# Kernel optimization log

Hardware: AMD Instinct MI355X
Metric: run time of the kernel (lower is better)

The kernel has to match this reference:

```python
import jax, jax.numpy as jnp
import numpy as np

IDENTITY_WEIGHT = 0.5
EPS_NORM = 1e-6   # channel RMSNorm eps
EPS_COS = 1e-12   # cosine-sim norm eps (matches torch F.normalize default)


def setup_inputs() -> dict:
    key = jax.random.key(0)
    k1, k2 = jax.random.split(key)
    B, C, H, W = 32, 768, 32, 32
    X = jax.random.normal(k1, (B, C, H, W), dtype=jnp.float32)
    # 1x1 conv weight [out=3C, in=C] (kernel dims squeezed)
    W_in = jax.random.normal(k2, (3 * C, C), dtype=jnp.float32) * (C ** -0.5)
    return {"X": X, "W_in": W_in}


def _cos_sim(t):
    # normalize over the flattened spatial axis (last dim)
    return t / (jnp.linalg.norm(t, axis=-1, keepdims=True) + EPS_COS)


def reference(X, W_in):
    B, C, H, W = X.shape
    # norm: parameter-free RMS over channel dim
    Xn = X * jax.lax.rsqrt(jnp.mean(X * X, axis=1, keepdims=True) + EPS_NORM)
    # 1x1 conv (bias-free) == channel GEMM: [B,3C,H,W]
    qkv = jnp.einsum('oc,bchw->bohw', W_in, Xn)
    K = qkv[:, :C].reshape(B, 1, C, H * W)       # b h c (x y), h=1
    V = qkv[:, C:2 * C].reshape(B, 1, C, H * W)
    # cosine similarity per channel over spatial positions: [B,1,C,1]
    A = jnp.sum(_cos_sim(K) * _cos_sim(V), axis=-1, keepdims=True)
    # affine gate with identity weight (feature_map_attn = identity)
    A = (1.0 - IDENTITY_WEIGHT) * A + IDENTITY_WEIGHT
    A = A.reshape(B, C, 1, 1)  # 'b 1 c 1 -> b c 1 1'
    return A * X
```

## Files before the change

### kernel.cpp

```cpp
#include <hip/hip_runtime.h>
#include <hip/hip_bf16.h>
#include <cstdint>
#include <cstddef>


#define B_   32
#define C_   768
#define HW_  1024
#define CHW_ (C_ * HW_)
#define EPS_NORM 1e-6f
#define EPS_COS  1e-12f

using f32x4  = __attribute__((ext_vector_type(4))) float;
using bf16x8 = __attribute__((ext_vector_type(8))) short;

__device__ inline unsigned short f2bf(float f) {
    union { float f; unsigned u; } v; v.f = f;
    unsigned u = v.u;
    u += 0x7fffu + ((u >> 16) & 1u);
    return (unsigned short)(u >> 16);
}

__global__ void sumsq_kernel(const float* __restrict__ X, float* __restrict__ ssum) {
    const int b  = blockIdx.z;
    const int hw = blockIdx.y * 256 + threadIdx.x;
    const int c0 = blockIdx.x * 128;
    const float* xp = X + (size_t)b * CHW_ + (size_t)c0 * HW_ + hw;
    float s = 0.f;
    #pragma unroll 8
    for (int c = 0; c < 128; ++c) {
        float v = xp[(size_t)c * HW_];
        s += v * v;
    }
    atomicAdd(&ssum[b * HW_ + hw], s);
}

__global__ void wconv_kernel(const float* __restrict__ W, unsigned short* __restrict__ Wbf) {
    const int i = blockIdx.x * 256 + threadIdx.x;
    const float4 v = reinterpret_cast<const float4*>(W)[i];
    ushort4 o;
    o.x = f2bf(v.x); o.y = f2bf(v.y); o.z = f2bf(v.z); o.w = f2bf(v.w);
    reinterpret_cast<ushort4*>(Wbf)[i] = o;
}

__global__ void xnt_kernel(const float* __restrict__ X, const float* __restrict__ ssum,
                           unsigned short* __restrict__ Xnt) {
    const int b   = blockIdx.z;
    const int c0  = blockIdx.y * 64;
    const int hw0 = blockIdx.x * 64;
    const int tid = threadIdx.x;
    __shared__ short T[64][72];

    #pragma unroll
    for (int it = 0; it < 4; ++it) {
        int q  = it * 256 + tid;
        int r  = q >> 4;
        int c4 = (q & 15) * 4;
        const float4 x = *reinterpret_cast<const float4*>(
            X + (size_t)b * CHW_ + (size_t)(c0 + r) * HW_ + hw0 + c4);
        const float4 s = *reinterpret_cast<const float4*>(ssum + b * HW_ + hw0 + c4);
        ushort4 o;
        o.x = f2bf(x.x * rsqrtf(s.x * (1.f / 768.f) + EPS_NORM));
        o.y = f2bf(x.y * rsqrtf(s.y * (1.f / 768.f) + EPS_NORM));
        o.z = f2bf(x.z * rsqrtf(s.z * (1.f / 768.f) + EPS_NORM));
        o.w = f2bf(x.w * rsqrtf(s.w * (1.f / 768.f) + EPS_NORM));
        *reinterpret_cast<ushort4*>(&T[r][c4]) = o;
    }
    __syncthreads();
    #pragma unroll
    for (int it = 0; it < 2; ++it) {
        int q  = it * 256 + tid;
        int rp = q >> 3;
        int cc = (q & 7) * 8;
        __align__(16) unsigned short tmp[8];
        #pragma unroll
        for (int j = 0; j < 8; ++j) tmp[j] = (unsigned short)T[cc + j][rp];
        *reinterpret_cast<uint4*>(
            Xnt + (size_t)b * CHW_ + (size_t)(hw0 + rp) * C_ + c0 + cc) =
            *reinterpret_cast<const uint4*>(tmp);
    }
}

__global__ __launch_bounds__(256, 2) void gemm_kernel(
        const unsigned short* __restrict__ Wbf,
        const unsigned short* __restrict__ Xnt,
        float* __restrict__ wsA) {
    const int n0   = blockIdx.x * 128;
    const int c0   = blockIdx.y * 128;
    const int b    = blockIdx.z;
    const int tid  = threadIdx.x;
    const int lane = tid & 63;
    const int wave = tid >> 6;
    const int wm   = (wave >> 1) * 64;
    const int wn   = (wave & 1) * 64;
    const int quad = lane >> 4;
    const int l15  = lane & 15;

    __shared__ short sAK[128][40];
    __shared__ short sAV[128][40];
    __shared__ short sB [128][40];

    const f32x4 zero = {0.f, 0.f, 0.f, 0.f};
    f32x4 accK[4][4], accV[4][4];
    #pragma unroll
    for (int i = 0; i < 4; ++i)
        #pragma unroll
        for (int j = 0; j < 4; ++j) { accK[i][j] = zero; accV[i][j] = zero; }

    const size_t wk_base = (size_t)c0 * 768;
    const size_t wv_base = (size_t)(768 + c0) * 768;
    const size_t xb      = (size_t)b * CHW_ + (size_t)n0 * 768;

    for (int k0 = 0; k0 < 768; k0 += 32) {
        __syncthreads();
        #pragma unroll
        for (int it = 0; it < 2; ++it) {
            int chunk = it * 256 + tid;
            int r  = chunk >> 2;
            int kk = (chunk & 3) * 8;
            uint4 vk = *reinterpret_cast<const uint4*>(Wbf + wk_base + (size_t)r * 768 + k0 + kk);
            *reinterpret_cast<uint4*>(&sAK[r][kk]) = vk;
            uint4 vv = *reinterpret_cast<const uint4*>(Wbf + wv_base + (size_t)r * 768 + k0 + kk);
            *reinterpret_cast<uint4*>(&sAV[r][kk]) = vv;
            uint4 vb = *reinterpret_cast<const uint4*>(Xnt + xb + (size_t)r * 768 + k0 + kk);
            *reinterpret_cast<uint4*>(&sB[r][kk]) = vb;
        }
        __syncthreads();

        bf16x8 aK[4], aV[4], bF[4];
        #pragma unroll
        for (int i = 0; i < 4; ++i) {
            aK[i] = *reinterpret_cast<const bf16x8*>(&sAK[wm + 16 * i + l15][quad * 8]);
            aV[i] = *reinterpret_cast<const bf16x8*>(&sAV[wm + 16 * i + l15][quad * 8]);
            bF[i] = *reinterpret_cast<const bf16x8*>(&sB [wn + 16 * i + l15][quad * 8]);
        }
        #pragma unroll
        for (int i = 0; i < 4; ++i)
            #pragma unroll
            for (int j = 0; j < 4; ++j) {
                accK[i][j] = __builtin_amdgcn_mfma_f32_16x16x32_bf16(aK[i], bF[j], accK[i][j], 0, 0, 0);
                accV[i][j] = __builtin_amdgcn_mfma_f32_16x16x32_bf16(aV[i], bF[j], accV[i][j], 0, 0, 0);
            }
    }

    #pragma unroll
    for (int i = 0; i < 4; ++i) {
        #pragma unroll
        for (int r = 0; r < 4; ++r) {
            float pd = 0.f, pk = 0.f, pv = 0.f;
            #pragma unroll
            for (int j = 0; j < 4; ++j) {
                float kk = accK[i][j][r], vv = accV[i][j][r];
                pd += kk * vv; pk += kk * kk; pv += vv * vv;
            }
            #pragma unroll
            for (int off = 1; off < 16; off <<= 1) {
                pd += __shfl_xor(pd, off);
                pk += __shfl_xor(pk, off);
                pv += __shfl_xor(pv, off);
            }
            if (l15 == 0) {
                int c = c0 + wm + 16 * i + 4 * quad + r;
                float* dst = wsA + ((size_t)b * C_ + c) * 3;
                atomicAdd(dst + 0, pd);
                atomicAdd(dst + 1, pk);
                atomicAdd(dst + 2, pv);
            }
        }
    }
}

__global__ void final_kernel(const float* __restrict__ X, const float* __restrict__ wsA,
                             float* __restrict__ out) {
    const int i4 = blockIdx.x * 256 + threadIdx.x;
    const size_t e = (size_t)i4 * 4;
    const int b = (int)(e / CHW_);
    const int c = (int)((e >> 10) % C_);
    const float* a = wsA + ((size_t)b * C_ + c) * 3;
    const float pd = a[0], pk = a[1], pv = a[2];
    const float A = pd / ((sqrtf(pk) + EPS_COS) * (sqrtf(pv) + EPS_COS));
    const float g = 0.5f * A + 0.5f;
    float4 x = reinterpret_cast<const float4*>(X)[i4];
    float4 o;
    o.x = x.x * g; o.y = x.y * g; o.z = x.z * g; o.w = x.w * g;
    reinterpret_cast<float4*>(out)[i4] = o;
}

extern "C" void kernel_launch(void* const* d_in, const int* in_sizes, int n_in,
                              void* d_out, int out_size, void* d_ws, size_t ws_size,
                              hipStream_t stream) {
    const float* X = (const float*)d_in[0];
    const float* W = (const float*)d_in[1];
    float* out = (float*)d_out;

    char* ws = (char*)d_ws;
    float* wsA           = (float*)ws;
    float* ssum          = (float*)(ws + 294912);
    unsigned short* Wbf  = (unsigned short*)(ws + 425984);
    unsigned short* Xnt  = (unsigned short*)(ws + 2785280);

    hipMemsetAsync(ws, 0, 425984, stream);

    sumsq_kernel<<<dim3(6, 4, 32),   256, 0, stream>>>(X, ssum);
    wconv_kernel<<<dim3(1152),       256, 0, stream>>>(W, Wbf);
    xnt_kernel  <<<dim3(16, 12, 32), 256, 0, stream>>>(X, ssum, Xnt);
    gemm_kernel <<<dim3(8, 6, 32),   256, 0, stream>>>(Wbf, Xnt, wsA);
    final_kernel<<<dim3(24576),      256, 0, stream>>>(X, wsA, out);
}
```

Baseline: 355.9 us.

## Fuse RMS sum-of-squares into transpose kernel; load GEMM tiles directly into swizzled LDS

The separate sum-of-squares kernel, its atomics and its workspace are removed. A single norm-transpose kernel per (batch, 64-position tile) now reduces the channel RMS in LDS, then loops over all 12 channel tiles to write the normalized bf16 transpose. The GEMM now stages its K, V and X tiles with global_load_lds 16-byte direct-to-LDS loads into unpadded tiles, using an XOR swizzle on the 8-element chunks to avoid bank conflicts. In exchange, the fused kernel launches far fewer blocks, each doing serial work over 12 tiles, which may reduce parallelism.

```diff
diff --git a/kernel.cpp b/kernel.cpp
--- a/kernel.cpp
+++ b/kernel.cpp
@@ -21,18 +21,11 @@
     return (unsigned short)(u >> 16);
 }
 
-__global__ void sumsq_kernel(const float* __restrict__ X, float* __restrict__ ssum) {
-    const int b  = blockIdx.z;
-    const int hw = blockIdx.y * 256 + threadIdx.x;
-    const int c0 = blockIdx.x * 128;
-    const float* xp = X + (size_t)b * CHW_ + (size_t)c0 * HW_ + hw;
-    float s = 0.f;
-    #pragma unroll 8
-    for (int c = 0; c < 128; ++c) {
-        float v = xp[(size_t)c * HW_];
-        s += v * v;
-    }
-    atomicAdd(&ssum[b * HW_ + hw], s);
+__device__ __forceinline__ void load16_lds(const unsigned short* g, short* l) {
+    __builtin_amdgcn_global_load_lds(
+        (const __attribute__((address_space(1))) unsigned int*)g,
+        (__attribute__((address_space(3))) unsigned int*)l,
+        16, 0, 0);
 }
 
 __global__ void wconv_kernel(const float* __restrict__ W, unsigned short* __restrict__ Wbf) {
@@ -43,41 +36,65 @@
     reinterpret_cast<ushort4*>(Wbf)[i] = o;
 }
 
-__global__ void xnt_kernel(const float* __restrict__ X, const float* __restrict__ ssum,
-                           unsigned short* __restrict__ Xnt) {
-    const int b   = blockIdx.z;
-    const int c0  = blockIdx.y * 64;
+__global__ __launch_bounds__(256) void normxnt_kernel(const float* __restrict__ X,
+                                                      unsigned short* __restrict__ Xnt) {
+    const int b   = blockIdx.y;
     const int hw0 = blockIdx.x * 64;
     const int tid = threadIdx.x;
+
+    __shared__ float red[4][64];
+    __shared__ float rstd[64];
     __shared__ short T[64][72];
 
-    #pragma unroll
-    for (int it = 0; it < 4; ++it) {
-        int q  = it * 256 + tid;
-        int r  = q >> 4;
-        int c4 = (q & 15) * 4;
-        const float4 x = *reinterpret_cast<const float4*>(
-            X + (size_t)b * CHW_ + (size_t)(c0 + r) * HW_ + hw0 + c4);
-        const float4 s = *reinterpret_cast<const float4*>(ssum + b * HW_ + hw0 + c4);
-        ushort4 o;
-        o.x = f2bf(x.x * rsqrtf(s.x * (1.f / 768.f) + EPS_NORM));
-        o.y = f2bf(x.y * rsqrtf(s.y * (1.f / 768.f) + EPS_NORM));
-        o.z = f2bf(x.z * rsqrtf(s.z * (1.f / 768.f) + EPS_NORM));
-        o.w = f2bf(x.w * rsqrtf(s.w * (1.f / 768.f) + EPS_NORM));
-        *reinterpret_cast<ushort4*>(&T[r][c4]) = o;
+    {
+        const int hwl = tid & 63;
+        const int cp  = tid >> 6;
+        const float* xp = X + (size_t)b * CHW_ + (size_t)(cp * 192) * HW_ + hw0 + hwl;
+        float s = 0.f;
+        #pragma unroll 8
+        for (int c = 0; c < 192; ++c) {
+            float v = xp[(size_t)c * HW_];
+            s += v * v;
+        }
+        red[cp][hwl] = s;
     }
     __syncthreads();
-    #pragma unroll
-    for (int it = 0; it < 2; ++it) {
-        int q  = it * 256 + tid;
-        int rp = q >> 3;
-        int cc = (q & 7) * 8;
-        __align__(16) unsigned short tmp[8];
-        #pragma unroll
-        for (int j = 0; j < 8; ++j) tmp[j] = (unsigned short)T[cc + j][rp];
-        *reinterpret_cast<uint4*>(
-            Xnt + (size_t)b * CHW_ + (size_t)(hw0 + rp) * C_ + c0 + cc) =
-            *reinterpret_cast<const uint4*>(tmp);
+    if (tid < 64) {
+        float t = red[0][tid] + red[1][tid] + red[2][tid] + red[3][tid];
+        rstd[tid] = rsqrtf(t * (1.f / 768.f) + EPS_NORM);
+    }
+    __syncthreads();
+
+    for (int ct = 0; ct < 12; ++ct) {
+        const int c0 = ct * 64;
+        #pragma unroll
+        for (int it = 0; it < 4; ++it) {
+            int q  = it * 256 + tid;
+            int r  = q >> 4;
+            int c4 = (q & 15) * 4;
+            const float4 x = *reinterpret_cast<const float4*>(
+                X + (size_t)b * CHW_ + (size_t)(c0 + r) * HW_ + hw0 + c4);
+            ushort4 o;
+            o.x = f2bf(x.x * rstd[c4 + 0]);
+            o.y = f2bf(x.y * rstd[c4 + 1]);
+            o.z = f2bf(x.z * rstd[c4 + 2]);
+            o.w = f2bf(x.w * rstd[c4 + 3]);
+            *reinterpret_cast<ushort4*>(&T[r][c4]) = o;
+        }
+        __syncthreads();
+        #pragma unroll
+        for (int it = 0; it < 2; ++it) {
+            int q  = it * 256 + tid;
+            int rp = q >> 3;
+            int cc = (q & 7) * 8;
+            __align__(16) unsigned short tmp[8];
+            #pragma unroll
+            for (int j = 0; j < 8; ++j) tmp[j] = (unsigned short)T[cc + j][rp];
+            *reinterpret_cast<uint4*>(
+                Xnt + (size_t)b * CHW_ + (size_t)(hw0 + rp) * C_ + c0 + cc) =
+                *reinterpret_cast<const uint4*>(tmp);
+        }
+        __syncthreads();
     }
 }
 
@@ -96,9 +113,9 @@
     const int quad = lane >> 4;
     const int l15  = lane & 15;
 
-    __shared__ short sAK[128][40];
-    __shared__ short sAV[128][40];
-    __shared__ short sB [128][40];
+    __shared__ short sAK[128][32];
+    __shared__ short sAV[128][32];
+    __shared__ short sB [128][32];
 
     const f32x4 zero = {0.f, 0.f, 0.f, 0.f};
     f32x4 accK[4][4], accV[4][4];
@@ -111,28 +128,37 @@
     const size_t wv_base = (size_t)(768 + c0) * 768;
     const size_t xb      = (size_t)b * CHW_ + (size_t)n0 * 768;
 
+    const int slot0   = tid;
+    const int row0    = slot0 >> 2;
+    const int chunk0  = (slot0 & 3) ^ ((row0 >> 1) & 3);
+    const int slot1   = 256 + tid;
+    const int row1    = slot1 >> 2;
+    const int chunk1  = (slot1 & 3) ^ ((row1 >> 1) & 3);
+    const int ldsrow0 = wave * 16;
+    const int ldsrow1 = 64 + wave * 16;
+    const size_t goff0 = (size_t)row0 * 768 + chunk0 * 8;
+    const size_t goff1 = (size_t)row1 * 768 + chunk1 * 8;
+
     for (int k0 = 0; k0 < 768; k0 += 32) {
         __syncthreads();
-        #pragma unroll
-        for (int it = 0; it < 2; ++it) {
-            int chunk = it * 256 + tid;
-            int r  = chunk >> 2;
-            int kk = (chunk & 3) * 8;
-            uint4 vk = *reinterpret_cast<const uint4*>(Wbf + wk_base + (size_t)r * 768 + k0 + kk);
-            *reinterpret_cast<uint4*>(&sAK[r][kk]) = vk;
-            uint4 vv = *reinterpret_cast<const uint4*>(Wbf + wv_base + (size_t)r * 768 + k0 + kk);
-            *reinterpret_cast<uint4*>(&sAV[r][kk]) = vv;
-            uint4 vb = *reinterpret_cast<const uint4*>(Xnt + xb + (size_t)r * 768 + k0 + kk);
-            *reinterpret_cast<uint4*>(&sB[r][kk]) = vb;
-        }
+        load16_lds(Wbf + wk_base + goff0 + k0, &sAK[ldsrow0][0]);
+        load16_lds(Wbf + wv_base + goff0 + k0, &sAV[ldsrow0][0]);
+        load16_lds(Xnt + xb      + goff0 + k0, &sB [ldsrow0][0]);
+        load16_lds(Wbf + wk_base + goff1 + k0, &sAK[ldsrow1][0]);
+        load16_lds(Wbf + wv_base + goff1 + k0, &sAV[ldsrow1][0]);
+        load16_lds(Xnt + xb      + goff1 + k0, &sB [ldsrow1][0]);
         __syncthreads();
 
         bf16x8 aK[4], aV[4], bF[4];
         #pragma unroll
         for (int i = 0; i < 4; ++i) {
-            aK[i] = *reinterpret_cast<const bf16x8*>(&sAK[wm + 16 * i + l15][quad * 8]);
-            aV[i] = *reinterpret_cast<const bf16x8*>(&sAV[wm + 16 * i + l15][quad * 8]);
-            bF[i] = *reinterpret_cast<const bf16x8*>(&sB [wn + 16 * i + l15][quad * 8]);
+            const int rA = wm + 16 * i + l15;
+            const int oA = ((((rA >> 1) & 3) ^ quad)) * 8;
+            aK[i] = *reinterpret_cast<const bf16x8*>(&sAK[rA][oA]);
+            aV[i] = *reinterpret_cast<const bf16x8*>(&sAV[rA][oA]);
+            const int rB = wn + 16 * i + l15;
+            const int oB = ((((rB >> 1) & 3) ^ quad)) * 8;
+            bF[i] = *reinterpret_cast<const bf16x8*>(&sB[rB][oB]);
         }
         #pragma unroll
         for (int i = 0; i < 4; ++i)
@@ -195,15 +221,13 @@
 
     char* ws = (char*)d_ws;
     float* wsA           = (float*)ws;
-    float* ssum          = (float*)(ws + 294912);
-    unsigned short* Wbf  = (unsigned short*)(ws + 425984);
-    unsigned short* Xnt  = (unsigned short*)(ws + 2785280);
-
-    hipMemsetAsync(ws, 0, 425984, stream);
-
-    sumsq_kernel<<<dim3(6, 4, 32),   256, 0, stream>>>(X, ssum);
-    wconv_kernel<<<dim3(1152),       256, 0, stream>>>(W, Wbf);
-    xnt_kernel  <<<dim3(16, 12, 32), 256, 0, stream>>>(X, ssum, Xnt);
-    gemm_kernel <<<dim3(8, 6, 32),   256, 0, stream>>>(Wbf, Xnt, wsA);
-    final_kernel<<<dim3(24576),      256, 0, stream>>>(X, wsA, out);
-}
+    unsigned short* Wbf  = (unsigned short*)(ws + 294912);
+    unsigned short* Xnt  = (unsigned short*)(ws + 2654208);
+
+    hipMemsetAsync(wsA, 0, 294912, stream);
+
+    wconv_kernel  <<<dim3(1152),      256, 0, stream>>>(W, Wbf);
+    normxnt_kernel<<<dim3(16, 32),    256, 0, stream>>>(X, Xnt);
+    gemm_kernel   <<<dim3(8, 6, 32),  256, 0, stream>>>(Wbf, Xnt, wsA);
+    final_kernel  <<<dim3(24576),     256, 0, stream>>>(X, wsA, out);
+}
```

Measured after the change: 349.8 us. No clear change (-1.7%).

## Use direct global-to-LDS loads with XOR swizzle and K=64 tiles in GEMM

Applied to the files above, without the earlier changes.

The GEMM now stages W and Xnt tiles with global_load_lds 16-byte direct loads into an XOR-swizzled 64-wide LDS layout and processes K in steps of 64, which halves the barrier count and removes register round-trips. The sumsq kernel is rewritten to use float4 loads over 32-channel slabs with more blocks, and final_kernel indexes per (b,c) block to avoid the divide and modulo. The xnt LDS padding is also changed. Risks are correctness of the swizzled direct-to-LDS addressing and more atomics in sumsq.

```diff
diff --git a/kernel.cpp b/kernel.cpp
--- a/kernel.cpp
+++ b/kernel.cpp
@@ -21,18 +21,11 @@
     return (unsigned short)(u >> 16);
 }
 
-__global__ void sumsq_kernel(const float* __restrict__ X, float* __restrict__ ssum) {
-    const int b  = blockIdx.z;
-    const int hw = blockIdx.y * 256 + threadIdx.x;
-    const int c0 = blockIdx.x * 128;
-    const float* xp = X + (size_t)b * CHW_ + (size_t)c0 * HW_ + hw;
-    float s = 0.f;
-    #pragma unroll 8
-    for (int c = 0; c < 128; ++c) {
-        float v = xp[(size_t)c * HW_];
-        s += v * v;
-    }
-    atomicAdd(&ssum[b * HW_ + hw], s);
+__device__ __forceinline__ void load16_lds(const unsigned short* g, short* l) {
+    __builtin_amdgcn_global_load_lds(
+        (const __attribute__((address_space(1))) unsigned int*)g,
+        (__attribute__((address_space(3))) unsigned int*)l,
+        16, 0, 0);
 }
 
 __global__ void wconv_kernel(const float* __restrict__ W, unsigned short* __restrict__ Wbf) {
@@ -43,13 +36,32 @@
     reinterpret_cast<ushort4*>(Wbf)[i] = o;
 }
 
-__global__ void xnt_kernel(const float* __restrict__ X, const float* __restrict__ ssum,
-                           unsigned short* __restrict__ Xnt) {
+__global__ void sumsq_kernel(const float* __restrict__ X, float* __restrict__ ssum) {
+    const int b  = blockIdx.y;
+    const int c0 = blockIdx.x * 32;
+    const int t  = threadIdx.x;
+    const float4* xp = reinterpret_cast<const float4*>(X + (size_t)b * CHW_ + (size_t)c0 * HW_) + t;
+    float4 s = {0.f, 0.f, 0.f, 0.f};
+    #pragma unroll 8
+    for (int c = 0; c < 32; ++c) {
+        float4 v = xp[c * 256];
+        s.x += v.x * v.x; s.y += v.y * v.y; s.z += v.z * v.z; s.w += v.w * v.w;
+    }
+    float* dst = ssum + b * HW_ + t * 4;
+    atomicAdd(dst + 0, s.x);
+    atomicAdd(dst + 1, s.y);
+    atomicAdd(dst + 2, s.z);
+    atomicAdd(dst + 3, s.w);
+}
+
+__global__ __launch_bounds__(256) void xnt_kernel(const float* __restrict__ X,
+                                                  const float* __restrict__ ssum,
+                                                  unsigned short* __restrict__ Xnt) {
     const int b   = blockIdx.z;
     const int c0  = blockIdx.y * 64;
     const int hw0 = blockIdx.x * 64;
     const int tid = threadIdx.x;
-    __shared__ short T[64][72];
+    __shared__ short T[64][78];
 
     #pragma unroll
     for (int it = 0; it < 4; ++it) {
@@ -96,9 +108,9 @@
     const int quad = lane >> 4;
     const int l15  = lane & 15;
 
-    __shared__ short sAK[128][40];
-    __shared__ short sAV[128][40];
-    __shared__ short sB [128][40];
+    __shared__ short sAK[128][64];
+    __shared__ short sAV[128][64];
+    __shared__ short sB [128][64];
 
     const f32x4 zero = {0.f, 0.f, 0.f, 0.f};
     f32x4 accK[4][4], accV[4][4];
@@ -111,36 +123,48 @@
     const size_t wv_base = (size_t)(768 + c0) * 768;
     const size_t xb      = (size_t)b * CHW_ + (size_t)n0 * 768;
 
-    for (int k0 = 0; k0 < 768; k0 += 32) {
+    size_t goff[4];
+    int    lrow[4];
+    #pragma unroll
+    for (int it = 0; it < 4; ++it) {
+        int q   = it * 256 + tid;
+        int row = q >> 3;
+        int gch = (q & 7) ^ (row & 7);
+        goff[it] = (size_t)row * 768 + gch * 8;
+        lrow[it] = row & ~7;
+    }
+
+    for (int k0 = 0; k0 < 768; k0 += 64) {
         __syncthreads();
         #pragma unroll
-        for (int it = 0; it < 2; ++it) {
-            int chunk = it * 256 + tid;
-            int r  = chunk >> 2;
-            int kk = (chunk & 3) * 8;
-            uint4 vk = *reinterpret_cast<const uint4*>(Wbf + wk_base + (size_t)r * 768 + k0 + kk);
-            *reinterpret_cast<uint4*>(&sAK[r][kk]) = vk;
-            uint4 vv = *reinterpret_cast<const uint4*>(Wbf + wv_base + (size_t)r * 768 + k0 + kk);
-            *reinterpret_cast<uint4*>(&sAV[r][kk]) = vv;
-            uint4 vb = *reinterpret_cast<const uint4*>(Xnt + xb + (size_t)r * 768 + k0 + kk);
-            *reinterpret_cast<uint4*>(&sB[r][kk]) = vb;
+        for (int it = 0; it < 4; ++it) {
+            load16_lds(Wbf + wk_base + goff[it] + k0, &sAK[lrow[it]][0]);
+            load16_lds(Wbf + wv_base + goff[it] + k0, &sAV[lrow[it]][0]);
+            load16_lds(Xnt + xb      + goff[it] + k0, &sB [lrow[it]][0]);
         }
         __syncthreads();
 
-        bf16x8 aK[4], aV[4], bF[4];
-        #pragma unroll
-        for (int i = 0; i < 4; ++i) {
-            aK[i] = *reinterpret_cast<const bf16x8*>(&sAK[wm + 16 * i + l15][quad * 8]);
-            aV[i] = *reinterpret_cast<const bf16x8*>(&sAV[wm + 16 * i + l15][quad * 8]);
-            bF[i] = *reinterpret_cast<const bf16x8*>(&sB [wn + 16 * i + l15][quad * 8]);
+        #pragma unroll
+        for (int kh = 0; kh < 2; ++kh) {
+            bf16x8 aK[4], aV[4], bF[4];
+            #pragma unroll
+            for (int i = 0; i < 4; ++i) {
+                const int rA = wm + 16 * i + l15;
+                const int sA = ((kh * 4 + quad) ^ (rA & 7)) * 8;
+                aK[i] = *reinterpret_cast<const bf16x8*>(&sAK[rA][sA]);
+                aV[i] = *reinterpret_cast<const bf16x8*>(&sAV[rA][sA]);
+                const int rB = wn + 16 * i + l15;
+                const int sBo = ((kh * 4 + quad) ^ (rB & 7)) * 8;
+                bF[i] = *reinterpret_cast<const bf16x8*>(&sB[rB][sBo]);
+            }
+            #pragma unroll
+            for (int i = 0; i < 4; ++i)
+                #pragma unroll
+                for (int j = 0; j < 4; ++j) {
+                    accK[i][j] = __builtin_amdgcn_mfma_f32_16x16x32_bf16(aK[i], bF[j], accK[i][j], 0, 0, 0);
+                    accV[i][j] = __builtin_amdgcn_mfma_f32_16x16x32_bf16(aV[i], bF[j], accV[i][j], 0, 0, 0);
+                }
         }
-        #pragma unroll
-        for (int i = 0; i < 4; ++i)
-            #pragma unroll
-            for (int j = 0; j < 4; ++j) {
-                accK[i][j] = __builtin_amdgcn_mfma_f32_16x16x32_bf16(aK[i], bF[j], accK[i][j], 0, 0, 0);
-                accV[i][j] = __builtin_amdgcn_mfma_f32_16x16x32_bf16(aV[i], bF[j], accV[i][j], 0, 0, 0);
-            }
     }
 
     #pragma unroll
@@ -172,14 +196,12 @@
 
 __global__ void final_kernel(const float* __restrict__ X, const float* __restrict__ wsA,
                              float* __restrict__ out) {
-    const int i4 = blockIdx.x * 256 + threadIdx.x;
-    const size_t e = (size_t)i4 * 4;
-    const int b = (int)(e / CHW_);
-    const int c = (int)((e >> 10) % C_);
-    const float* a = wsA + ((size_t)b * C_ + c) * 3;
+    const int bc = blockIdx.x;
+    const float* a = wsA + (size_t)bc * 3;
     const float pd = a[0], pk = a[1], pv = a[2];
     const float A = pd / ((sqrtf(pk) + EPS_COS) * (sqrtf(pv) + EPS_COS));
     const float g = 0.5f * A + 0.5f;
+    const size_t i4 = (size_t)bc * 256 + threadIdx.x;
     float4 x = reinterpret_cast<const float4*>(X)[i4];
     float4 o;
     o.x = x.x * g; o.y = x.y * g; o.z = x.z * g; o.w = x.w * g;
@@ -201,8 +223,8 @@
 
     hipMemsetAsync(ws, 0, 425984, stream);
 
-    sumsq_kernel<<<dim3(6, 4, 32),   256, 0, stream>>>(X, ssum);
     wconv_kernel<<<dim3(1152),       256, 0, stream>>>(W, Wbf);
+    sumsq_kernel<<<dim3(24, 32),     256, 0, stream>>>(X, ssum);
     xnt_kernel  <<<dim3(16, 12, 32), 256, 0, stream>>>(X, ssum, Xnt);
     gemm_kernel <<<dim3(8, 6, 32),   256, 0, stream>>>(Wbf, Xnt, wsA);
     final_kernel<<<dim3(24576),      256, 0, stream>>>(X, wsA, out);
```

Result: faster. 335.2 us (-5.8%).
